# Kernel tuning notes

Hardware: AMD Instinct MI355X
Metric: run time of the kernel (lower is better)

## Reference

```python
import jax, jax.numpy as jnp
import numpy as np


def fake_quant(w, bits):
    # Symmetric per-tensor fake quantization with straight-through estimator.
    qmax = 2.0 ** (bits - 1) - 1.0
    scale = jnp.max(jnp.abs(w)) / qmax
    wq = jnp.clip(jnp.round(w / scale), -qmax, qmax) * scale
    return w + jax.lax.stop_gradient(wq - w)


def setup_inputs() -> dict:
    key = jax.random.key(0)
    k = jax.random.split(key, 5)
    B, S, D, H = 64, 196, 768, 3072
    x = jax.random.normal(k[0], (B, S, D), dtype=jnp.float32)
    w1 = jax.random.normal(k[1], (H, D), dtype=jnp.float32) * (1.0 / np.sqrt(D))
    b1 = jax.random.normal(k[2], (H,), dtype=jnp.float32) * 0.01
    w2 = jax.random.normal(k[3], (D, H), dtype=jnp.float32) * (1.0 / np.sqrt(H))
    b2 = jax.random.normal(k[4], (D,), dtype=jnp.float32) * 0.01
    return {"x": x, "w1": w1, "b1": b1, "w2": w2, "b2": b2, "bits": 8}


def reference(x, w1, b1, w2, b2, bits):
    # fc1 (fake-quant weight) -> ReLU -> fc2 (fake-quant weight)
    w1q = fake_quant(w1, bits)
    w2q = fake_quant(w2, bits)
    h = jnp.einsum('bsd,hd->bsh', x, w1q) + b1   # [B,S,3072]
    h = jax.nn.relu(h)
    out = jnp.einsum('bsh,dh->bsd', h, w2q) + b2  # [B,S,768]
    return out
```

## Files before the change

kernel.cpp:

```cpp
#include <hip/hip_runtime.h>
#include <hip/hip_bf16.h>
#include <stdint.h>

typedef __attribute__((ext_vector_type(8))) short bf16x8;
typedef __attribute__((ext_vector_type(4))) float f32x4;

__device__ __forceinline__ unsigned short f2bf(float f) {
  __hip_bfloat16 h = __float2bfloat16(f);
  return *reinterpret_cast<unsigned short*>(&h);
}

__global__ void absmax2_kernel(const float* __restrict__ w1, const float* __restrict__ w2,
                               int n4, unsigned int* __restrict__ out) {
  const float* w = blockIdx.y ? w2 : w1;
  __shared__ unsigned int red[256];
  unsigned int m = 0u;
  const uint4* w4 = reinterpret_cast<const uint4*>(w);
  for (int i = blockIdx.x * blockDim.x + threadIdx.x; i < n4;
       i += gridDim.x * blockDim.x) {
    uint4 v = w4[i];
    m = max(m, v.x & 0x7fffffffu);
    m = max(m, v.y & 0x7fffffffu);
    m = max(m, v.z & 0x7fffffffu);
    m = max(m, v.w & 0x7fffffffu);
  }
  red[threadIdx.x] = m;
  __syncthreads();
  for (int s = 128; s > 0; s >>= 1) {
    if ((int)threadIdx.x < s)
      red[threadIdx.x] = max(red[threadIdx.x], red[threadIdx.x + s]);
    __syncthreads();
  }
  if (threadIdx.x == 0) atomicMax(out + blockIdx.y, red[0]);
}

__global__ void quant2_kernel(const float* __restrict__ w1, const float* __restrict__ w2,
                              int n4, const unsigned int* __restrict__ maxbits,
                              const int* __restrict__ bits,
                              unsigned short* __restrict__ o1, unsigned short* __restrict__ o2) {
  const float* w = blockIdx.y ? w2 : w1;
  unsigned short* o = blockIdx.y ? o2 : o1;
  const float qmax = (float)((1 << (*bits - 1)) - 1);
  const float scale = __uint_as_float(maxbits[blockIdx.y]) / qmax;
  const float4* w4 = reinterpret_cast<const float4*>(w);
  ushort4* o4 = reinterpret_cast<ushort4*>(o);
  for (int i = blockIdx.x * blockDim.x + threadIdx.x; i < n4;
       i += gridDim.x * blockDim.x) {
    float4 v = w4[i];
    float a = fminf(fmaxf(rintf(v.x / scale), -qmax), qmax) * scale;
    float b = fminf(fmaxf(rintf(v.y / scale), -qmax), qmax) * scale;
    float c = fminf(fmaxf(rintf(v.z / scale), -qmax), qmax) * scale;
    float d = fminf(fmaxf(rintf(v.w / scale), -qmax), qmax) * scale;
    o4[i] = make_ushort4(f2bf(a), f2bf(b), f2bf(c), f2bf(d));
  }
}

__global__ void cast_kernel(const float* __restrict__ x, int n4,
                            unsigned short* __restrict__ out) {
  const float4* x4 = reinterpret_cast<const float4*>(x);
  ushort4* o4 = reinterpret_cast<ushort4*>(out);
  for (int i = blockIdx.x * blockDim.x + threadIdx.x; i < n4;
       i += gridDim.x * blockDim.x) {
    float4 v = x4[i];
    o4[i] = make_ushort4(f2bf(v.x), f2bf(v.y), f2bf(v.z), f2bf(v.w));
  }
}

template<int BM, bool RELU, bool BF16_OUT>
__global__ __launch_bounds__(256)
void gemm_bt(const unsigned short* __restrict__ A,
             const unsigned short* __restrict__ B,
             const float* __restrict__ bias,
             void* __restrict__ Cout,
             int M, int N, int K, int gx) {
  constexpr int BK = 64;
  constexpr int MF = BM / 32;
  __shared__ __attribute__((aligned(16))) unsigned short As[2][BM * BK];
  __shared__ __attribute__((aligned(16))) unsigned short Bs[2][128 * BK];

  const int nwg = gridDim.x;
  const int orig = blockIdx.x;
  const int q = nwg >> 3, r = nwg & 7;
  const int xcd = orig & 7, cidx = orig >> 3;
  const int wgid = (xcd < r ? xcd * (q + 1) : r * (q + 1) + (xcd - r) * q) + cidx;
  const int bx = wgid % gx;
  const int by = wgid / gx;

  const int tid = threadIdx.x;
  const int lane = tid & 63;
  const int wave = tid >> 6;
  const int wr = wave >> 1;
  const int wc = wave & 1;
  const long brow = (long)by * BM;
  const long bcol = (long)bx * 128;

  f32x4 acc[MF][4] = {};

  const int srow = lane >> 3;
  const int gslot = ((lane & 7) ^ (lane >> 3)) * 8;
  const int fr = lane & 15;
  const int fs = lane >> 4;

  auto stage = [&](int k0, int b) {
#pragma unroll
    for (int it = 0; it < BM / 32; ++it) {
      const int c = it * 4 + wave;
      const unsigned short* ga = A + (brow + c * 8 + srow) * (long)K + k0 + gslot;
      __builtin_amdgcn_global_load_lds(
          (const __attribute__((address_space(1))) void*)ga,
          (__attribute__((address_space(3))) void*)(&As[b][c * 512]), 16, 0, 0);
    }
#pragma unroll
    for (int it = 0; it < 4; ++it) {
      const int c = it * 4 + wave;
      const unsigned short* gb = B + (bcol + c * 8 + srow) * (long)K + k0 + gslot;
      __builtin_amdgcn_global_load_lds(
          (const __attribute__((address_space(1))) void*)gb,
          (__attribute__((address_space(3))) void*)(&Bs[b][c * 512]), 16, 0, 0);
    }
  };

  const int nt = K / BK;
  stage(0, 0);
  stage(BK, 1);

  for (int t = 0; t < nt; ++t) {
    const int b = t & 1;
    if (t < nt - 1) {
      if constexpr (BM == 128) asm volatile("s_waitcnt vmcnt(8)" ::: "memory");
      else                     asm volatile("s_waitcnt vmcnt(6)" ::: "memory");
    } else {
      asm volatile("s_waitcnt vmcnt(0)" ::: "memory");
    }
    __builtin_amdgcn_s_barrier();

    const unsigned short* as = &As[b][0];
    const unsigned short* bs = &Bs[b][0];
#pragma unroll
    for (int kk = 0; kk < 2; ++kk) {
      const int s = kk * 4 + fs;
      bf16x8 a[MF], bb[4];
#pragma unroll
      for (int m = 0; m < MF; ++m) {
        const int row = wr * (MF * 16) + m * 16 + fr;
        a[m] = *reinterpret_cast<const bf16x8*>(as + row * BK + ((s ^ (row & 7)) * 8));
      }
#pragma unroll
      for (int n = 0; n < 4; ++n) {
        const int row = wc * 64 + n * 16 + fr;
        bb[n] = *reinterpret_cast<const bf16x8*>(bs + row * BK + ((s ^ (row & 7)) * 8));
      }
#pragma unroll
      for (int m = 0; m < MF; ++m)
#pragma unroll
        for (int n = 0; n < 4; ++n)
          acc[m][n] = __builtin_amdgcn_mfma_f32_16x16x32_bf16(a[m], bb[n], acc[m][n], 0, 0, 0);
    }

    asm volatile("s_waitcnt lgkmcnt(0)" ::: "memory");
    __builtin_amdgcn_sched_barrier(0);
    __builtin_amdgcn_s_barrier();
    if (t + 2 < nt) stage((t + 2) * BK, b);
  }

  const int fq = lane >> 4;
#pragma unroll
  for (int n = 0; n < 4; ++n) {
    const long col = bcol + wc * 64 + n * 16 + fr;
    const float bv = bias[col];
#pragma unroll
    for (int m = 0; m < MF; ++m) {
#pragma unroll
      for (int rr = 0; rr < 4; ++rr) {
        const long row = brow + wr * (MF * 16) + m * 16 + fq * 4 + rr;
        float v = acc[m][n][rr] + bv;
        if (RELU) v = fmaxf(v, 0.0f);
        if (BF16_OUT)
          ((unsigned short*)Cout)[row * N + col] = f2bf(v);
        else
          ((float*)Cout)[row * N + col] = v;
      }
    }
  }
}

extern "C" void kernel_launch(void* const* d_in, const int* in_sizes, int n_in,
                              void* d_out, int out_size, void* d_ws, size_t ws_size,
                              hipStream_t stream) {
  const float* x  = (const float*)d_in[0];
  const float* w1 = (const float*)d_in[1];
  const float* b1 = (const float*)d_in[2];
  const float* w2 = (const float*)d_in[3];
  const float* b2 = (const float*)d_in[4];
  const int* bits = (const int*)d_in[5];

  const int M = 64 * 196;
  const int D = 768, H = 3072;
  const int nx = M * D;
  const int nw1 = H * D;
  const int nw2 = D * H;

  char* ws = (char*)d_ws;
  unsigned int* scales = (unsigned int*)ws;
  unsigned short* xb  = (unsigned short*)(ws + 256);
  unsigned short* w1q = (unsigned short*)(ws + 256 + (size_t)nx * 2);
  unsigned short* w2q = (unsigned short*)(ws + 256 + (size_t)nx * 2 + (size_t)nw1 * 2);
  unsigned short* hb  = (unsigned short*)(ws + 256 + (size_t)nx * 2 + (size_t)(nw1 + nw2) * 2);

  hipMemsetAsync(scales, 0, 8, stream);
  absmax2_kernel<<<dim3(512, 2), 256, 0, stream>>>(w1, w2, nw1 / 4, scales);
  quant2_kernel<<<dim3(512, 2), 256, 0, stream>>>(w1, w2, nw1 / 4, scales, bits, w1q, w2q);
  cast_kernel<<<2048, 256, 0, stream>>>(x, nx / 4, xb);

  gemm_bt<128, true, true><<<(H / 128) * (M / 128), 256, 0, stream>>>(
      xb, w1q, b1, hb, M, H, D, H / 128);
  gemm_bt<64, false, false><<<(D / 128) * (M / 64), 256, 0, stream>>>(
      hb, w2q, b2, d_out, M, D, H, D / 128);
}
```

Baseline: 197.3 us.

## Halve GEMM K-tile to raise occupancy and fuse quant with cast kernel

```diff
diff --git a/kernel.cpp b/kernel.cpp
--- a/kernel.cpp
+++ b/kernel.cpp
@@ -34,17 +34,31 @@
   if (threadIdx.x == 0) atomicMax(out + blockIdx.y, red[0]);
 }
 
-__global__ void quant2_kernel(const float* __restrict__ w1, const float* __restrict__ w2,
-                              int n4, const unsigned int* __restrict__ maxbits,
-                              const int* __restrict__ bits,
-                              unsigned short* __restrict__ o1, unsigned short* __restrict__ o2) {
+__global__ void quantcast_kernel(const float* __restrict__ w1, const float* __restrict__ w2,
+                                 const float* __restrict__ x,
+                                 int n4w, int n4x,
+                                 const unsigned int* __restrict__ maxbits,
+                                 const int* __restrict__ bits,
+                                 unsigned short* __restrict__ o1,
+                                 unsigned short* __restrict__ o2,
+                                 unsigned short* __restrict__ ox) {
+  if (blockIdx.y == 2) {
+    const float4* x4 = reinterpret_cast<const float4*>(x);
+    ushort4* o4 = reinterpret_cast<ushort4*>(ox);
+    for (int i = blockIdx.x * blockDim.x + threadIdx.x; i < n4x;
+         i += gridDim.x * blockDim.x) {
+      float4 v = x4[i];
+      o4[i] = make_ushort4(f2bf(v.x), f2bf(v.y), f2bf(v.z), f2bf(v.w));
+    }
+    return;
+  }
   const float* w = blockIdx.y ? w2 : w1;
   unsigned short* o = blockIdx.y ? o2 : o1;
   const float qmax = (float)((1 << (*bits - 1)) - 1);
   const float scale = __uint_as_float(maxbits[blockIdx.y]) / qmax;
   const float4* w4 = reinterpret_cast<const float4*>(w);
   ushort4* o4 = reinterpret_cast<ushort4*>(o);
-  for (int i = blockIdx.x * blockDim.x + threadIdx.x; i < n4;
+  for (int i = blockIdx.x * blockDim.x + threadIdx.x; i < n4w;
        i += gridDim.x * blockDim.x) {
     float4 v = w4[i];
     float a = fminf(fmaxf(rintf(v.x / scale), -qmax), qmax) * scale;
@@ -55,25 +69,14 @@
   }
 }
 
-__global__ void cast_kernel(const float* __restrict__ x, int n4,
-                            unsigned short* __restrict__ out) {
-  const float4* x4 = reinterpret_cast<const float4*>(x);
-  ushort4* o4 = reinterpret_cast<ushort4*>(out);
-  for (int i = blockIdx.x * blockDim.x + threadIdx.x; i < n4;
-       i += gridDim.x * blockDim.x) {
-    float4 v = x4[i];
-    o4[i] = make_ushort4(f2bf(v.x), f2bf(v.y), f2bf(v.z), f2bf(v.w));
-  }
-}
-
-template<int BM, bool RELU, bool BF16_OUT>
-__global__ __launch_bounds__(256)
+template<int BM, int MINW, bool RELU, bool BF16_OUT>
+__global__ __launch_bounds__(256, MINW)
 void gemm_bt(const unsigned short* __restrict__ A,
              const unsigned short* __restrict__ B,
              const float* __restrict__ bias,
              void* __restrict__ Cout,
              int M, int N, int K, int gx) {
-  constexpr int BK = 64;
+  constexpr int BK = 32;
   constexpr int MF = BM / 32;
   __shared__ __attribute__((aligned(16))) unsigned short As[2][BM * BK];
   __shared__ __attribute__((aligned(16))) unsigned short Bs[2][128 * BK];
@@ -96,24 +99,24 @@
 
   f32x4 acc[MF][4] = {};
 
-  const int srow = lane >> 3;
-  const int gslot = ((lane & 7) ^ (lane >> 3)) * 8;
+  const int srow = lane >> 2;
+  const int gslot = ((lane & 3) ^ ((lane >> 3) & 3)) * 8;
   const int fr = lane & 15;
   const int fs = lane >> 4;
 
   auto stage = [&](int k0, int b) {
 #pragma unroll
-    for (int it = 0; it < BM / 32; ++it) {
+    for (int it = 0; it < BM / 64; ++it) {
       const int c = it * 4 + wave;
-      const unsigned short* ga = A + (brow + c * 8 + srow) * (long)K + k0 + gslot;
+      const unsigned short* ga = A + (brow + c * 16 + srow) * (long)K + k0 + gslot;
       __builtin_amdgcn_global_load_lds(
           (const __attribute__((address_space(1))) void*)ga,
           (__attribute__((address_space(3))) void*)(&As[b][c * 512]), 16, 0, 0);
     }
 #pragma unroll
-    for (int it = 0; it < 4; ++it) {
+    for (int it = 0; it < 2; ++it) {
       const int c = it * 4 + wave;
-      const unsigned short* gb = B + (bcol + c * 8 + srow) * (long)K + k0 + gslot;
+      const unsigned short* gb = B + (bcol + c * 16 + srow) * (long)K + k0 + gslot;
       __builtin_amdgcn_global_load_lds(
           (const __attribute__((address_space(1))) void*)gb,
           (__attribute__((address_space(3))) void*)(&Bs[b][c * 512]), 16, 0, 0);
@@ -127,8 +130,8 @@
   for (int t = 0; t < nt; ++t) {
     const int b = t & 1;
     if (t < nt - 1) {
-      if constexpr (BM == 128) asm volatile("s_waitcnt vmcnt(8)" ::: "memory");
-      else                     asm volatile("s_waitcnt vmcnt(6)" ::: "memory");
+      if constexpr (BM == 128) asm volatile("s_waitcnt vmcnt(4)" ::: "memory");
+      else                     asm volatile("s_waitcnt vmcnt(3)" ::: "memory");
     } else {
       asm volatile("s_waitcnt vmcnt(0)" ::: "memory");
     }
@@ -136,26 +139,22 @@
 
     const unsigned short* as = &As[b][0];
     const unsigned short* bs = &Bs[b][0];
-#pragma unroll
-    for (int kk = 0; kk < 2; ++kk) {
-      const int s = kk * 4 + fs;
-      bf16x8 a[MF], bb[4];
-#pragma unroll
-      for (int m = 0; m < MF; ++m) {
-        const int row = wr * (MF * 16) + m * 16 + fr;
-        a[m] = *reinterpret_cast<const bf16x8*>(as + row * BK + ((s ^ (row & 7)) * 8));
-      }
-#pragma unroll
-      for (int n = 0; n < 4; ++n) {
-        const int row = wc * 64 + n * 16 + fr;
-        bb[n] = *reinterpret_cast<const bf16x8*>(bs + row * BK + ((s ^ (row & 7)) * 8));
-      }
-#pragma unroll
-      for (int m = 0; m < MF; ++m)
-#pragma unroll
-        for (int n = 0; n < 4; ++n)
-          acc[m][n] = __builtin_amdgcn_mfma_f32_16x16x32_bf16(a[m], bb[n], acc[m][n], 0, 0, 0);
-    }
+    bf16x8 a[MF], bb[4];
+#pragma unroll
+    for (int m = 0; m < MF; ++m) {
+      const int row = wr * (MF * 16) + m * 16 + fr;
+      a[m] = *reinterpret_cast<const bf16x8*>(as + row * BK + ((fs ^ ((row >> 1) & 3)) * 8));
+    }
+#pragma unroll
+    for (int n = 0; n < 4; ++n) {
+      const int row = wc * 64 + n * 16 + fr;
+      bb[n] = *reinterpret_cast<const bf16x8*>(bs + row * BK + ((fs ^ ((row >> 1) & 3)) * 8));
+    }
+#pragma unroll
+    for (int m = 0; m < MF; ++m)
+#pragma unroll
+      for (int n = 0; n < 4; ++n)
+        acc[m][n] = __builtin_amdgcn_mfma_f32_16x16x32_bf16(a[m], bb[n], acc[m][n], 0, 0, 0);
 
     asm volatile("s_waitcnt lgkmcnt(0)" ::: "memory");
     __builtin_amdgcn_sched_barrier(0);
@@ -209,11 +208,11 @@
 
   hipMemsetAsync(scales, 0, 8, stream);
   absmax2_kernel<<<dim3(512, 2), 256, 0, stream>>>(w1, w2, nw1 / 4, scales);
-  quant2_kernel<<<dim3(512, 2), 256, 0, stream>>>(w1, w2, nw1 / 4, scales, bits, w1q, w2q);
-  cast_kernel<<<2048, 256, 0, stream>>>(x, nx / 4, xb);
-
-  gemm_bt<128, true, true><<<(H / 128) * (M / 128), 256, 0, stream>>>(
+  quantcast_kernel<<<dim3(768, 3), 256, 0, stream>>>(w1, w2, x, nw1 / 4, nx / 4,
+                                                     scales, bits, w1q, w2q, xb);
+
+  gemm_bt<128, 5, true, true><<<(H / 128) * (M / 128), 256, 0, stream>>>(
       xb, w1q, b1, hb, M, H, D, H / 128);
-  gemm_bt<64, false, false><<<(D / 128) * (M / 64), 256, 0, stream>>>(
+  gemm_bt<64, 6, false, false><<<(D / 128) * (M / 64), 256, 0, stream>>>(
       hb, w2q, b2, d_out, M, D, H, D / 128);
 }
```

Result: slower. 232.2 us (+17.7%).
